# Optimization experiments

Measured on AMD Instinct MI355X. Metric: run time of the kernel, lower is better.

## Reference

```python
import jax, jax.numpy as jnp
import numpy as np

NY, NX = 1024, 2048
DX, DT, NU, UB = 1.0, 0.1, 0.01, 1.0
NITER = 5
NLEVEL = int(np.log2(NY)) + 1  # 11
DIAG = -8.0 / (3.0 * DX * DX)  # center coefficient of the Laplacian stencil wA


def _conv(x, w, stride=1):
    # single-channel 'VALID' cross-correlation, same semantics as torch Conv2d(padding=0)
    return jax.lax.conv_general_dilated(x, w, (stride, stride), 'VALID',
                                        dimension_numbers=('NCHW', 'OIHW', 'NCHW'))


def _bc_u(u):
    # inlet (left/top/bottom) = ub, zero-gradient outflow on the right
    uu = jnp.pad(u, ((0, 0), (0, 0), (1, 1), (1, 1)))
    uu = uu.at[:, :, :, 0].set(UB)
    uu = uu.at[:, :, :, -1].set(uu[:, :, :, -2])
    uu = uu.at[:, :, 0, :].set(UB)
    uu = uu.at[:, :, -1, :].set(UB)
    return uu


def _bc_v(v):
    # v = 0 on inlet/top/bottom (zero pad), zero-gradient outflow on the right
    vv = jnp.pad(v, ((0, 0), (0, 0), (1, 1), (1, 1)))
    vv = vv.at[:, :, :, -1].set(vv[:, :, :, -2])
    return vv


def _bc_p(p):
    # zero-gradient pressure except fixed p=0 at the outlet
    pp = jnp.pad(p, ((0, 0), (0, 0), (1, 1), (1, 1)))
    pp = pp.at[:, :, :, 0].set(pp[:, :, :, 1])
    pp = pp.at[:, :, :, -1].set(0.0)
    pp = pp.at[:, :, 0, :].set(pp[:, :, 1, :])
    pp = pp.at[:, :, -1, :].set(pp[:, :, -2, :])
    return pp


def _bc_cw(a):
    # homogeneous (zero) halo for the multigrid correction
    return jnp.pad(a, ((0, 0), (0, 0), (1, 1), (1, 1)))


def _prolong(a):
    return jnp.repeat(jnp.repeat(a, 2, axis=2), 2, axis=3)


def _f_cycle_mg(uu, vv, p, w_xadv, w_yadv, w_A, w_res):
    b = -(_conv(uu, w_xadv) + _conv(vv, w_yadv)) / DT
    for _ in range(NITER):
        r = _conv(_bc_p(p), w_A) - b
        r_s = [r]
        for _i in range(1, NLEVEL):
            r = _conv(r, w_res, stride=2)
            r_s.append(r)
        a = jnp.zeros((1, 1, 1, 1), dtype=p.dtype)
        for i in reversed(range(1, NLEVEL)):
            if i == NLEVEL - 1:
                a = r_s[i] / DIAG
            else:
                a = a - _conv(_bc_cw(a), w_A) / DIAG + r_s[i] / DIAG
            a = _prolong(a)
        p = p - a
        p = p - _conv(_bc_p(p), w_A) / DIAG + b / DIAG
    return p


def _forward(u, v, p, sigma, w_xadv, w_yadv, w_diff, w_A, w_res):
    uu, vv, pp = _bc_u(u), _bc_v(v), _bc_p(p)
    Grapx_p = _conv(pp, w_xadv) * DT
    Grapy_p = _conv(pp, w_yadv) * DT
    ADx_u, ADy_u = _conv(uu, w_xadv), _conv(uu, w_yadv)
    ADx_v, ADy_v = _conv(vv, w_xadv), _conv(vv, w_yadv)
    AD2_u, AD2_v = _conv(uu, w_diff), _conv(vv, w_diff)
    # predictor half-step
    bu = u + 0.5 * (NU * AD2_u * DT - u * ADx_u * DT - v * ADy_u * DT) - Grapx_p
    bv = v + 0.5 * (NU * AD2_v * DT - u * ADx_v * DT - v * ADy_v * DT) - Grapy_p
    damp = 1.0 / (1.0 + DT * sigma)  # solid body Brinkman penalty
    bu, bv = bu * damp, bv * damp
    buu, bvv = _bc_u(bu), _bc_v(bv)
    ADx_u, ADy_u = _conv(buu, w_xadv), _conv(buu, w_yadv)
    ADx_v, ADy_v = _conv(bvv, w_xadv), _conv(bvv, w_yadv)
    AD2_u, AD2_v = _conv(buu, w_diff), _conv(bvv, w_diff)
    # corrector step
    u = u + NU * AD2_u * DT - bu * ADx_u * DT - bv * ADy_u * DT - Grapx_p
    v = v + NU * AD2_v * DT - bu * ADx_v * DT - bv * ADy_v * DT - Grapy_p
    u, v = u * damp, v * damp
    uu, vv = _bc_u(u), _bc_v(v)
    # pressure solve via multigrid F-cycle + projection
    p = _f_cycle_mg(uu, vv, p, w_xadv, w_yadv, w_A, w_res)
    pp = _bc_p(p)
    u = u - _conv(pp, w_xadv) * DT
    v = v - _conv(pp, w_yadv) * DT
    u, v = u * damp, v * damp
    return jnp.concatenate([u, v, p], axis=1)  # (1, 3, NY, NX)


def setup_inputs() -> dict:
    key = jax.random.key(0)
    k1, k2, k3 = jax.random.split(key, 3)
    shp = (1, 1, NY, NX)
    u = jax.random.normal(k1, shp, jnp.float32) * 0.1 + UB
    v = jax.random.normal(k2, shp, jnp.float32) * 0.1
    p = jax.random.normal(k3, shp, jnp.float32) * 0.1
    # bluff-body mask: 1/timescale inside the rectangle (Block.create_solid_body_2D)
    cor_x, cor_y = NX // 4, NY // 2
    size_x, size_y = NX // 32, NY // 8
    sigma = jnp.zeros(shp, jnp.float32)
    sigma = sigma.at[0, 0, cor_y - size_y:cor_y + size_y,
                     cor_x - size_x:cor_x + size_x].set(1e8)
    # finite-difference stencils from get_weights_linear_2D(dx)
    w_diff = jnp.array([[1., 1., 1.], [1., -8., 1.], [1., 1., 1.]],
                       jnp.float32).reshape(1, 1, 3, 3) / (3.0 * DX * DX)
    w_xadv = jnp.array([[-1., 0., 1.], [-4., 0., 4.], [-1., 0., 1.]],
                       jnp.float32).reshape(1, 1, 3, 3) / (12.0 * DX)
    w_yadv = jnp.array([[-1., -4., -1.], [0., 0., 0.], [1., 4., 1.]],
                       jnp.float32).reshape(1, 1, 3, 3) / (12.0 * DX)
    w_A = w_diff
    w_res = jnp.full((1, 1, 2, 2), 0.25, jnp.float32)
    return {"u": u, "v": v, "p": p, "sigma": sigma, "w_xadv": w_xadv,
            "w_yadv": w_yadv, "w_diff": w_diff, "w_A": w_A, "w_res": w_res}


def reference(u, v, p, sigma, w_xadv, w_yadv, w_diff, w_A, w_res):
    return _forward(u, v, p, sigma, w_xadv, w_yadv, w_diff, w_A, w_res)
```

## Files before the change

### kernel.cpp

```cpp
#include <hip/hip_runtime.h>
#include <cstdint>

#define GNY 1024
#define GNX 2048
#define GNPTS (GNY * GNX)

namespace {
constexpr float DT = 0.1f;
constexpr float NUc = 0.01f;
constexpr float INV_DIAG = -0.375f;
}

__device__ __forceinline__ float bc_u_at(const float* __restrict__ f, int y, int x) {
    if (y < 0 || y >= GNY || x < 0) return 1.0f;
    if (x >= GNX) x = GNX - 1;
    return f[y * GNX + x];
}
__device__ __forceinline__ float bc_v_at(const float* __restrict__ f, int y, int x) {
    if (y < 0 || y >= GNY || x < 0) return 0.0f;
    if (x >= GNX) x = GNX - 1;
    return f[y * GNX + x];
}
__device__ __forceinline__ float bc_p_at(const float* __restrict__ f, int y, int x) {
    if (x >= GNX) return 0.0f;
    if (x < 0) x = 0;
    y = min(max(y, 0), GNY - 1);
    return f[y * GNX + x];
}

__device__ __forceinline__ float conv_x3(const float m[3][3]) {
    return ((m[0][2] - m[0][0]) + 4.0f * (m[1][2] - m[1][0]) + (m[2][2] - m[2][0])) * (1.0f / 12.0f);
}
__device__ __forceinline__ float conv_y3(const float m[3][3]) {
    return ((m[2][0] - m[0][0]) + 4.0f * (m[2][1] - m[0][1]) + (m[2][2] - m[0][2])) * (1.0f / 12.0f);
}
__device__ __forceinline__ float conv_d3(const float m[3][3]) {
    return (m[0][0] + m[0][1] + m[0][2] + m[1][0] + m[1][2] + m[2][0] + m[2][1] + m[2][2]
            - 8.0f * m[1][1]) * (1.0f / 3.0f);
}

template <typename PG>
__device__ __forceinline__ float up_val(PG pget, float rval, int H, int W, int y, int x) {
    float m[3][3];
#pragma unroll
    for (int dy = 0; dy < 3; ++dy)
#pragma unroll
        for (int dx = 0; dx < 3; ++dx) {
            int yy = y + dy - 1, xx = x + dx - 1;
            m[dy][dx] = (yy >= 0 && yy < H && xx >= 0 && xx < W) ? pget(yy >> 1, xx >> 1) : 0.0f;
        }
    float conv = (m[0][0] + m[0][1] + m[0][2] + m[1][0] + m[1][2]
                  + m[2][0] + m[2][1] + m[2][2] - 8.0f * m[1][1]) * (1.0f / 3.0f);
    return m[1][1] - conv * INV_DIAG + rval * INV_DIAG;
}

__global__ __launch_bounds__(256) void k_predict(
        const float* __restrict__ u, const float* __restrict__ v,
        const float* __restrict__ p, const float* __restrict__ sigma,
        float* __restrict__ bu, float* __restrict__ bv) {
    int x = blockIdx.x * blockDim.x + threadIdx.x;
    int y = blockIdx.y * blockDim.y + threadIdx.y;
    if (x >= GNX || y >= GNY) return;
    float un[3][3], vn[3][3], pn[3][3];
#pragma unroll
    for (int dy = 0; dy < 3; ++dy)
#pragma unroll
        for (int dx = 0; dx < 3; ++dx) {
            int yy = y + dy - 1, xx = x + dx - 1;
            un[dy][dx] = bc_u_at(u, yy, xx);
            vn[dy][dx] = bc_v_at(v, yy, xx);
            pn[dy][dx] = bc_p_at(p, yy, xx);
        }
    float gx = conv_x3(pn) * DT, gy = conv_y3(pn) * DT;
    float uc = un[1][1], vc = vn[1][1];
    float damp = 1.0f / (1.0f + DT * sigma[y * GNX + x]);
    float bu_ = uc + 0.5f * (NUc * conv_d3(un) * DT - uc * conv_x3(un) * DT - vc * conv_y3(un) * DT) - gx;
    float bv_ = vc + 0.5f * (NUc * conv_d3(vn) * DT - uc * conv_x3(vn) * DT - vc * conv_y3(vn) * DT) - gy;
    bu[y * GNX + x] = bu_ * damp;
    bv[y * GNX + x] = bv_ * damp;
}

__global__ __launch_bounds__(256) void k_correct(
        const float* __restrict__ u, const float* __restrict__ v,
        const float* __restrict__ p, const float* __restrict__ sigma,
        const float* __restrict__ bu, const float* __restrict__ bv,
        float* __restrict__ u2, float* __restrict__ v2) {
    int x = blockIdx.x * blockDim.x + threadIdx.x;
    int y = blockIdx.y * blockDim.y + threadIdx.y;
    if (x >= GNX || y >= GNY) return;
    float bun[3][3], bvn[3][3], pn[3][3];
#pragma unroll
    for (int dy = 0; dy < 3; ++dy)
#pragma unroll
        for (int dx = 0; dx < 3; ++dx) {
            int yy = y + dy - 1, xx = x + dx - 1;
            bun[dy][dx] = bc_u_at(bu, yy, xx);
            bvn[dy][dx] = bc_v_at(bv, yy, xx);
            pn[dy][dx] = bc_p_at(p, yy, xx);
        }
    float gx = conv_x3(pn) * DT, gy = conv_y3(pn) * DT;
    float buc = bun[1][1], bvc = bvn[1][1];
    int idx = y * GNX + x;
    float damp = 1.0f / (1.0f + DT * sigma[idx]);
    float un_ = u[idx] + NUc * conv_d3(bun) * DT - buc * conv_x3(bun) * DT - bvc * conv_y3(bun) * DT - gx;
    float vn_ = v[idx] + NUc * conv_d3(bvn) * DT - buc * conv_x3(bvn) * DT - bvc * conv_y3(bvn) * DT - gy;
    u2[idx] = un_ * damp;
    v2[idx] = vn_ * damp;
}

__global__ __launch_bounds__(256) void k_rhs(
        const float* __restrict__ u2, const float* __restrict__ v2, float* __restrict__ b) {
    int x = blockIdx.x * blockDim.x + threadIdx.x;
    int y = blockIdx.y * blockDim.y + threadIdx.y;
    if (x >= GNX || y >= GNY) return;
    float un[3][3], vn[3][3];
#pragma unroll
    for (int dy = 0; dy < 3; ++dy)
#pragma unroll
        for (int dx = 0; dx < 3; ++dx) {
            int yy = y + dy - 1, xx = x + dx - 1;
            un[dy][dx] = bc_u_at(u2, yy, xx);
            vn[dy][dx] = bc_v_at(v2, yy, xx);
        }
    b[y * GNX + x] = -(conv_x3(un) + conv_y3(vn)) * (1.0f / DT);
}

__global__ __launch_bounds__(256) void k_resid_restrict(
        const float* __restrict__ p, const float* __restrict__ b,
        float* __restrict__ r1, float* __restrict__ r2, float* __restrict__ r3,
        float* __restrict__ r4, float* __restrict__ r5) {
    __shared__ float s0[32][33];
    __shared__ float s1[16][17];
    __shared__ float s2[8][9];
    __shared__ float s3[4][5];
    __shared__ float s4[2][3];
    int t = threadIdx.x;
    int tx = t & 31, tg = t >> 5;
    int x0 = blockIdx.x * 32, y0 = blockIdx.y * 32;
    int x = x0 + tx;
#pragma unroll
    for (int ry = 0; ry < 4; ++ry) {
        int yr = tg * 4 + ry;
        int y = y0 + yr;
        float pn[3][3];
#pragma unroll
        for (int dy = 0; dy < 3; ++dy)
#pragma unroll
            for (int dx = 0; dx < 3; ++dx)
                pn[dy][dx] = bc_p_at(p, y + dy - 1, x + dx - 1);
        s0[yr][tx] = conv_d3(pn) - b[y * GNX + x];
    }
    __syncthreads();
    {   int qy = t >> 4, qx = t & 15;
        float v = 0.25f * (s0[2*qy][2*qx] + s0[2*qy][2*qx+1] + s0[2*qy+1][2*qx] + s0[2*qy+1][2*qx+1]);
        s1[qy][qx] = v;
        r1[(blockIdx.y * 16 + qy) * 1024 + blockIdx.x * 16 + qx] = v; }
    __syncthreads();
    if (t < 64) { int qy = t >> 3, qx = t & 7;
        float v = 0.25f * (s1[2*qy][2*qx] + s1[2*qy][2*qx+1] + s1[2*qy+1][2*qx] + s1[2*qy+1][2*qx+1]);
        s2[qy][qx] = v;
        r2[(blockIdx.y * 8 + qy) * 512 + blockIdx.x * 8 + qx] = v; }
    __syncthreads();
    if (t < 16) { int qy = t >> 2, qx = t & 3;
        float v = 0.25f * (s2[2*qy][2*qx] + s2[2*qy][2*qx+1] + s2[2*qy+1][2*qx] + s2[2*qy+1][2*qx+1]);
        s3[qy][qx] = v;
        r3[(blockIdx.y * 4 + qy) * 256 + blockIdx.x * 4 + qx] = v; }
    __syncthreads();
    if (t < 4) { int qy = t >> 1, qx = t & 1;
        float v = 0.25f * (s3[2*qy][2*qx] + s3[2*qy][2*qx+1] + s3[2*qy+1][2*qx] + s3[2*qy+1][2*qx+1]);
        s4[qy][qx] = v;
        r4[(blockIdx.y * 2 + qy) * 128 + blockIdx.x * 2 + qx] = v; }
    __syncthreads();
    if (t == 0)
        r5[blockIdx.y * 64 + blockIdx.x] = 0.25f * (s4[0][0] + s4[0][1] + s4[1][0] + s4[1][1]);
}

__global__ __launch_bounds__(256) void k_mg(
        const float* __restrict__ p_src, const float* __restrict__ b,
        const float* __restrict__ r1, const float* __restrict__ r2,
        const float* __restrict__ r3, const float* __restrict__ r4,
        const float* __restrict__ r5,
        float* __restrict__ p_dst,
        float* __restrict__ o1, float* __restrict__ o2, float* __restrict__ o3,
        float* __restrict__ o4, float* __restrict__ o5,
        const float* __restrict__ sigma, float* __restrict__ u_io,
        float* __restrict__ v_io, int last) {
    __shared__ float scr[3948];
    __shared__ float w6v[9], w5v[9], w4v[16], w3v[36], w2v[100], w1v[324];
    float* s5  = scr;
    float* s6  = scr + 2048;
    float* s7  = scr + 2560;
    float* s8  = scr + 2688;
    float* s9  = scr + 2720;
    float* s10 = scr + 2728;
    float* a9  = scr + 2730;
    float* a8  = scr + 2738;
    float* a7  = scr + 2770;
    float* sPp = scr;
    float* sPn = scr + 1332;
    float* s0  = scr + 2522;
    float* s1  = scr + 3578;
    float* s2  = scr + 3850;
    float* s3  = scr + 3922;
    float* s4  = scr + 3942;

    int t = threadIdx.x;
    int bx = blockIdx.x, by = blockIdx.y;
    int y0 = by * 32, x0 = bx * 32;

    for (int i = t; i < 2048; i += 256) s5[i] = r5[i];
    __syncthreads();
    for (int i = t; i < 512; i += 256) {
        int y = i >> 5, x = i & 31;
        s6[i] = 0.25f * (s5[(2*y)*64 + 2*x] + s5[(2*y)*64 + 2*x + 1]
                       + s5[(2*y+1)*64 + 2*x] + s5[(2*y+1)*64 + 2*x + 1]);
    }
    __syncthreads();
    if (t < 128) { int y = t >> 4, x = t & 15;
        s7[t] = 0.25f * (s6[(2*y)*32 + 2*x] + s6[(2*y)*32 + 2*x + 1]
                       + s6[(2*y+1)*32 + 2*x] + s6[(2*y+1)*32 + 2*x + 1]); }
    __syncthreads();
    if (t < 32) { int y = t >> 3, x = t & 7;
        s8[t] = 0.25f * (s7[(2*y)*16 + 2*x] + s7[(2*y)*16 + 2*x + 1]
                       + s7[(2*y+1)*16 + 2*x] + s7[(2*y+1)*16 + 2*x + 1]); }
    __syncthreads();
    if (t < 8) { int y = t >> 2, x = t & 3;
        s9[t] = 0.25f * (s8[(2*y)*8 + 2*x] + s8[(2*y)*8 + 2*x + 1]
                       + s8[(2*y+1)*8 + 2*x] + s8[(2*y+1)*8 + 2*x + 1]); }
    __syncthreads();
    if (t < 2)
        s10[t] = 0.25f * (s9[2*t] + s9[2*t + 1] + s9[4 + 2*t] + s9[4 + 2*t + 1]);
    __syncthreads();
    if (t < 8) { int y = t >> 2, x = t & 3;
        a9[t] = up_val([&](int py, int px) { return s10[py*2 + px] * INV_DIAG; },
                       s9[t], 2, 4, y, x); }
    __syncthreads();
    if (t < 32) { int y = t >> 3, x = t & 7;
        a8[t] = up_val([&](int py, int px) { return a9[py*4 + px]; },
                       s8[t], 4, 8, y, x); }
    __syncthreads();
    if (t < 128) { int y = t >> 4, x = t & 15;
        a7[t] = up_val([&](int py, int px) { return a8[py*8 + px]; },
                       s7[t], 8, 16, y, x); }
    __syncthreads();

    int w6ylo = (by - 2) >> 1, w6xlo = (bx - 2) >> 1;
    int w5ylo = by - 1,        w5xlo = bx - 1;
    int w4ylo = 2*by - 1,      w4xlo = 2*bx - 1;
    int w3ylo = 4*by - 1,      w3xlo = 4*bx - 1;
    int w2ylo = 8*by - 1,      w2xlo = 8*bx - 1;
    int w1ylo = 16*by - 1,     w1xlo = 16*bx - 1;

    if (t < 9) { int gy = w6ylo + t/3, gx = w6xlo + t%3;
        w6v[t] = (gy >= 0 && gy < 16 && gx >= 0 && gx < 32)
            ? up_val([&](int py, int px) { return a7[py*16 + px]; },
                     s6[gy*32 + gx], 16, 32, gy, gx) : 0.0f; }
    __syncthreads();
    if (t < 9) { int gy = w5ylo + t/3, gx = w5xlo + t%3;
        w5v[t] = (gy >= 0 && gy < 32 && gx >= 0 && gx < 64)
            ? up_val([&](int py, int px) { return w6v[(py - w6ylo)*3 + (px - w6xlo)]; },
                     s5[gy*64 + gx], 32, 64, gy, gx) : 0.0f; }
    __syncthreads();
    if (t < 16) { int gy = w4ylo + t/4, gx = w4xlo + t%4;
        w4v[t] = (gy >= 0 && gy < 64 && gx >= 0 && gx < 128)
            ? up_val([&](int py, int px) { return w5v[(py - w5ylo)*3 + (px - w5xlo)]; },
                     r4[gy*128 + gx], 64, 128, gy, gx) : 0.0f; }
    __syncthreads();
    if (t < 36) { int gy = w3ylo + t/6, gx = w3xlo + t%6;
        w3v[t] = (gy >= 0 && gy < 128 && gx >= 0 && gx < 256)
            ? up_val([&](int py, int px) { return w4v[(py - w4ylo)*4 + (px - w4xlo)]; },
                     r3[gy*256 + gx], 128, 256, gy, gx) : 0.0f; }
    __syncthreads();
    if (t < 100) { int gy = w2ylo + t/10, gx = w2xlo + t%10;
        w2v[t] = (gy >= 0 && gy < 256 && gx >= 0 && gx < 512)
            ? up_val([&](int py, int px) { return w3v[(py - w3ylo)*6 + (px - w3xlo)]; },
                     r2[gy*512 + gx], 256, 512, gy, gx) : 0.0f; }
    __syncthreads();
    for (int i = t; i < 324; i += 256) { int gy = w1ylo + i/18, gx = w1xlo + i%18;
        w1v[i] = (gy >= 0 && gy < 512 && gx >= 0 && gx < 1024)
            ? up_val([&](int py, int px) { return w2v[(py - w2ylo)*10 + (px - w2xlo)]; },
                     r1[gy*1024 + gx], 512, 1024, gy, gx) : 0.0f; }
    __syncthreads();

    for (int i = t; i < 1296; i += 256) {
        int wy = i / 36, wx = i % 36;
        int gy = y0 - 2 + wy, gx = x0 - 2 + wx;
        float v = 0.0f;
        if (gy >= 0 && gy < GNY && gx >= 0 && gx < GNX)
            v = p_src[gy*GNX + gx] - w1v[((gy >> 1) - w1ylo)*18 + ((gx >> 1) - w1xlo)];
        sPp[wy*37 + wx] = v;
    }
    __syncthreads();
    for (int i = t; i < 1156; i += 256) {
        int wy = i / 34, wx = i % 34;
        int gy = y0 - 1 + wy, gx = x0 - 1 + wx;
        float v = 0.0f;
        if (gy >= 0 && gy < GNY && gx >= 0 && gx < GNX) {
            float m[3][3];
#pragma unroll
            for (int dy = 0; dy < 3; ++dy)
#pragma unroll
                for (int dx = 0; dx < 3; ++dx) {
                    int yy = gy + dy - 1, xx = gx + dx - 1;
                    float tv;
                    if (xx >= GNX) tv = 0.0f;
                    else {
                        int cx = xx < 0 ? 0 : xx;
                        int cy = min(max(yy, 0), GNY - 1);
                        tv = sPp[(cy - (y0 - 2))*37 + (cx - (x0 - 2))];
                    }
                    m[dy][dx] = tv;
                }
            float conv = (m[0][0] + m[0][1] + m[0][2] + m[1][0] + m[1][2]
                          + m[2][0] + m[2][1] + m[2][2] - 8.0f*m[1][1]) * (1.0f / 3.0f);
            v = m[1][1] - conv * INV_DIAG + b[gy*GNX + gx] * INV_DIAG;
        }
        sPn[wy*35 + wx] = v;
    }
    __syncthreads();
    for (int i = t; i < 1024; i += 256) {
        int ty = i >> 5, tx = i & 31;
        p_dst[(y0 + ty)*GNX + x0 + tx] = sPn[(ty + 1)*35 + (tx + 1)];
    }

    if (!last) {
        for (int i = t; i < 1024; i += 256) {
            int ty = i >> 5, tx = i & 31;
            int gy = y0 + ty, gx = x0 + tx;
            float m[3][3];
#pragma unroll
            for (int dy = 0; dy < 3; ++dy)
#pragma unroll
                for (int dx = 0; dx < 3; ++dx) {
                    int yy = gy + dy - 1, xx = gx + dx - 1;
                    float tv;
                    if (xx >= GNX) tv = 0.0f;
                    else {
                        int cx = xx < 0 ? 0 : xx;
                        int cy = min(max(yy, 0), GNY - 1);
                        tv = sPn[(cy - (y0 - 1))*35 + (cx - (x0 - 1))];
                    }
                    m[dy][dx] = tv;
                }
            s0[ty*33 + tx] = conv_d3(m) - b[gy*GNX + gx];
        }
        __syncthreads();
        { int qy = t >> 4, qx = t & 15;
          float v = 0.25f * (s0[(2*qy)*33 + 2*qx] + s0[(2*qy)*33 + 2*qx + 1]
                           + s0[(2*qy+1)*33 + 2*qx] + s0[(2*qy+1)*33 + 2*qx + 1]);
          s1[qy*17 + qx] = v;
          o1[(by*16 + qy)*1024 + bx*16 + qx] = v; }
        __syncthreads();
        if (t < 64) { int qy = t >> 3, qx = t & 7;
          float v = 0.25f * (s1[(2*qy)*17 + 2*qx] + s1[(2*qy)*17 + 2*qx + 1]
                           + s1[(2*qy+1)*17 + 2*qx] + s1[(2*qy+1)*17 + 2*qx + 1]);
          s2[qy*9 + qx] = v;
          o2[(by*8 + qy)*512 + bx*8 + qx] = v; }
        __syncthreads();
        if (t < 16) { int qy = t >> 2, qx = t & 3;
          float v = 0.25f * (s2[(2*qy)*9 + 2*qx] + s2[(2*qy)*9 + 2*qx + 1]
                           + s2[(2*qy+1)*9 + 2*qx] + s2[(2*qy+1)*9 + 2*qx + 1]);
          s3[qy*5 + qx] = v;
          o3[(by*4 + qy)*256 + bx*4 + qx] = v; }
        __syncthreads();
        if (t < 4) { int qy = t >> 1, qx = t & 1;
          float v = 0.25f * (s3[(2*qy)*5 + 2*qx] + s3[(2*qy)*5 + 2*qx + 1]
                           + s3[(2*qy+1)*5 + 2*qx] + s3[(2*qy+1)*5 + 2*qx + 1]);
          s4[qy*3 + qx] = v;
          o4[(by*2 + qy)*128 + bx*2 + qx] = v; }
        __syncthreads();
        if (t == 0)
            o5[by*64 + bx] = 0.25f * (s4[0] + s4[1] + s4[3] + s4[4]);
    } else {
        for (int i = t; i < 1024; i += 256) {
            int ty = i >> 5, tx = i & 31;
            int gy = y0 + ty, gx = x0 + tx;
            float m[3][3];
#pragma unroll
            for (int dy = 0; dy < 3; ++dy)
#pragma unroll
                for (int dx = 0; dx < 3; ++dx) {
                    int yy = gy + dy - 1, xx = gx + dx - 1;
                    float tv;
                    if (xx >= GNX) tv = 0.0f;
                    else {
                        int cx = xx < 0 ? 0 : xx;
                        int cy = min(max(yy, 0), GNY - 1);
                        tv = sPn[(cy - (y0 - 1))*35 + (cx - (x0 - 1))];
                    }
                    m[dy][dx] = tv;
                }
            int idx = gy*GNX + gx;
            float damp = 1.0f / (1.0f + DT * sigma[idx]);
            u_io[idx] = (u_io[idx] - conv_x3(m) * DT) * damp;
            v_io[idx] = (v_io[idx] - conv_y3(m) * DT) * damp;
        }
    }
}

extern "C" void kernel_launch(void* const* d_in, const int* in_sizes, int n_in,
                              void* d_out, int out_size, void* d_ws, size_t ws_size,
                              hipStream_t stream) {
    (void)in_sizes; (void)n_in; (void)out_size; (void)ws_size;
    const float* u_in  = (const float*)d_in[0];
    const float* v_in  = (const float*)d_in[1];
    const float* p_in  = (const float*)d_in[2];
    const float* sigma = (const float*)d_in[3];

    float* out_u = (float*)d_out;
    float* out_v = out_u + GNPTS;
    float* out_p = out_u + 2 * (size_t)GNPTS;

    float* ws   = (float*)d_ws;
    float* bu   = ws;
    float* bv   = bu + (size_t)GNPTS;
    float* b    = bv + (size_t)GNPTS;
    float* p_ws = b  + (size_t)GNPTS;
    float* base = p_ws + (size_t)GNPTS;
    float* A_[5], * B_[5];
    size_t lsz[5] = {524288, 131072, 32768, 8192, 2048};
    float* cur = base;
    for (int l = 0; l < 5; ++l) { A_[l] = cur; cur += lsz[l]; }
    for (int l = 0; l < 5; ++l) { B_[l] = cur; cur += lsz[l]; }

    dim3 blk2(64, 4), grd2(GNX / 64, GNY / 4);
    dim3 grdT(GNX / 32, GNY / 32), blkT(256);

    k_predict<<<grd2, blk2, 0, stream>>>(u_in, v_in, p_in, sigma, bu, bv);
    k_correct<<<grd2, blk2, 0, stream>>>(u_in, v_in, p_in, sigma, bu, bv, out_u, out_v);
    k_rhs<<<grd2, blk2, 0, stream>>>(out_u, out_v, b);

    k_resid_restrict<<<grdT, blkT, 0, stream>>>(p_in, b, A_[0], A_[1], A_[2], A_[3], A_[4]);

    const float* p_cur = p_in;
    float* p_bufs[2] = { out_p, p_ws };
    for (int it = 0; it < 5; ++it) {
        float** rp = (it % 2 == 0) ? A_ : B_;
        float** wp = (it % 2 == 0) ? B_ : A_;
        float* p_next = p_bufs[it % 2];
        int last = (it == 4) ? 1 : 0;
        k_mg<<<grdT, blkT, 0, stream>>>(p_cur, b,
                                        rp[0], rp[1], rp[2], rp[3], rp[4],
                                        p_next,
                                        wp[0], wp[1], wp[2], wp[3], wp[4],
                                        sigma, out_u, out_v, last);
        p_cur = p_next;
    }
}
```

Before: 239.0 us.

## Fuse predictor, corrector, RHS and restriction into one halo-recompute kernel

Merges the four front-end kernels (predict, correct, divergence RHS, residual+restriction) into a single tiled kernel. Each 32x32 tile recomputes bu/bv on a 2-cell halo and u2/v2 on a 1-cell halo in shared memory, so the bu/bv intermediates never touch global memory and three launches are dropped. The cost is redundant halo computation (about 27% extra for bu/bv) and heavy shared-memory use that may reduce occupancy.

Measured after the change: 240.3 us. No clear change (+0.5%).

```diff
diff --git a/kernel.cpp b/kernel.cpp
--- a/kernel.cpp
+++ b/kernel.cpp
@@ -54,125 +54,138 @@
     return m[1][1] - conv * INV_DIAG + rval * INV_DIAG;
 }
 
-__global__ __launch_bounds__(256) void k_predict(
+__global__ __launch_bounds__(256) void k_front(
         const float* __restrict__ u, const float* __restrict__ v,
         const float* __restrict__ p, const float* __restrict__ sigma,
-        float* __restrict__ bu, float* __restrict__ bv) {
-    int x = blockIdx.x * blockDim.x + threadIdx.x;
-    int y = blockIdx.y * blockDim.y + threadIdx.y;
-    if (x >= GNX || y >= GNY) return;
-    float un[3][3], vn[3][3], pn[3][3];
-#pragma unroll
-    for (int dy = 0; dy < 3; ++dy)
-#pragma unroll
-        for (int dx = 0; dx < 3; ++dx) {
-            int yy = y + dy - 1, xx = x + dx - 1;
-            un[dy][dx] = bc_u_at(u, yy, xx);
-            vn[dy][dx] = bc_v_at(v, yy, xx);
-            pn[dy][dx] = bc_p_at(p, yy, xx);
-        }
-    float gx = conv_x3(pn) * DT, gy = conv_y3(pn) * DT;
-    float uc = un[1][1], vc = vn[1][1];
-    float damp = 1.0f / (1.0f + DT * sigma[y * GNX + x]);
-    float bu_ = uc + 0.5f * (NUc * conv_d3(un) * DT - uc * conv_x3(un) * DT - vc * conv_y3(un) * DT) - gx;
-    float bv_ = vc + 0.5f * (NUc * conv_d3(vn) * DT - uc * conv_x3(vn) * DT - vc * conv_y3(vn) * DT) - gy;
-    bu[y * GNX + x] = bu_ * damp;
-    bv[y * GNX + x] = bv_ * damp;
-}
-
-__global__ __launch_bounds__(256) void k_correct(
-        const float* __restrict__ u, const float* __restrict__ v,
-        const float* __restrict__ p, const float* __restrict__ sigma,
-        const float* __restrict__ bu, const float* __restrict__ bv,
-        float* __restrict__ u2, float* __restrict__ v2) {
-    int x = blockIdx.x * blockDim.x + threadIdx.x;
-    int y = blockIdx.y * blockDim.y + threadIdx.y;
-    if (x >= GNX || y >= GNY) return;
-    float bun[3][3], bvn[3][3], pn[3][3];
-#pragma unroll
-    for (int dy = 0; dy < 3; ++dy)
-#pragma unroll
-        for (int dx = 0; dx < 3; ++dx) {
-            int yy = y + dy - 1, xx = x + dx - 1;
-            bun[dy][dx] = bc_u_at(bu, yy, xx);
-            bvn[dy][dx] = bc_v_at(bv, yy, xx);
-            pn[dy][dx] = bc_p_at(p, yy, xx);
-        }
-    float gx = conv_x3(pn) * DT, gy = conv_y3(pn) * DT;
-    float buc = bun[1][1], bvc = bvn[1][1];
-    int idx = y * GNX + x;
-    float damp = 1.0f / (1.0f + DT * sigma[idx]);
-    float un_ = u[idx] + NUc * conv_d3(bun) * DT - buc * conv_x3(bun) * DT - bvc * conv_y3(bun) * DT - gx;
-    float vn_ = v[idx] + NUc * conv_d3(bvn) * DT - buc * conv_x3(bvn) * DT - bvc * conv_y3(bvn) * DT - gy;
-    u2[idx] = un_ * damp;
-    v2[idx] = vn_ * damp;
-}
-
-__global__ __launch_bounds__(256) void k_rhs(
-        const float* __restrict__ u2, const float* __restrict__ v2, float* __restrict__ b) {
-    int x = blockIdx.x * blockDim.x + threadIdx.x;
-    int y = blockIdx.y * blockDim.y + threadIdx.y;
-    if (x >= GNX || y >= GNY) return;
-    float un[3][3], vn[3][3];
-#pragma unroll
-    for (int dy = 0; dy < 3; ++dy)
-#pragma unroll
-        for (int dx = 0; dx < 3; ++dx) {
-            int yy = y + dy - 1, xx = x + dx - 1;
-            un[dy][dx] = bc_u_at(u2, yy, xx);
-            vn[dy][dx] = bc_v_at(v2, yy, xx);
-        }
-    b[y * GNX + x] = -(conv_x3(un) + conv_y3(vn)) * (1.0f / DT);
-}
-
-__global__ __launch_bounds__(256) void k_resid_restrict(
-        const float* __restrict__ p, const float* __restrict__ b,
+        float* __restrict__ u2g, float* __restrict__ v2g, float* __restrict__ bg,
         float* __restrict__ r1, float* __restrict__ r2, float* __restrict__ r3,
         float* __restrict__ r4, float* __restrict__ r5) {
-    __shared__ float s0[32][33];
-    __shared__ float s1[16][17];
-    __shared__ float s2[8][9];
-    __shared__ float s3[4][5];
-    __shared__ float s4[2][3];
+    __shared__ float sBu[36 * 37], sBv[36 * 37];
+    __shared__ float sU2[34 * 35], sV2[34 * 35];
+    __shared__ float s0[32 * 33];
+    __shared__ float s1[16 * 17];
+    __shared__ float s2[8 * 9];
+    __shared__ float s3[4 * 5];
+    __shared__ float s4[2 * 3];
+
     int t = threadIdx.x;
-    int tx = t & 31, tg = t >> 5;
-    int x0 = blockIdx.x * 32, y0 = blockIdx.y * 32;
-    int x = x0 + tx;
-#pragma unroll
-    for (int ry = 0; ry < 4; ++ry) {
-        int yr = tg * 4 + ry;
-        int y = y0 + yr;
-        float pn[3][3];
+    int bx = blockIdx.x, by = blockIdx.y;
+    int y0 = by * 32, x0 = bx * 32;
+
+    for (int i = t; i < 1296; i += 256) {
+        int wy = i / 36, wx = i - wy * 36;
+        int gy = y0 - 2 + wy, gx = x0 - 2 + wx;
+        float bu_ = 0.0f, bv_ = 0.0f;
+        if (gy >= 0 && gy < GNY && gx >= 0 && gx < GNX) {
+            float un[3][3], vn[3][3], pn[3][3];
+#pragma unroll
+            for (int dy = 0; dy < 3; ++dy)
+#pragma unroll
+                for (int dx = 0; dx < 3; ++dx) {
+                    int yy = gy + dy - 1, xx = gx + dx - 1;
+                    un[dy][dx] = bc_u_at(u, yy, xx);
+                    vn[dy][dx] = bc_v_at(v, yy, xx);
+                    pn[dy][dx] = bc_p_at(p, yy, xx);
+                }
+            float gxp = conv_x3(pn) * DT, gyp = conv_y3(pn) * DT;
+            float uc = un[1][1], vc = vn[1][1];
+            float damp = 1.0f / (1.0f + DT * sigma[gy * GNX + gx]);
+            bu_ = (uc + 0.5f * (NUc * conv_d3(un) * DT - uc * conv_x3(un) * DT - vc * conv_y3(un) * DT) - gxp) * damp;
+            bv_ = (vc + 0.5f * (NUc * conv_d3(vn) * DT - uc * conv_x3(vn) * DT - vc * conv_y3(vn) * DT) - gyp) * damp;
+        }
+        sBu[wy * 37 + wx] = bu_;
+        sBv[wy * 37 + wx] = bv_;
+    }
+    __syncthreads();
+
+    for (int i = t; i < 1156; i += 256) {
+        int wy = i / 34, wx = i - wy * 34;
+        int gy = y0 - 1 + wy, gx = x0 - 1 + wx;
+        float u2_ = 0.0f, v2_ = 0.0f;
+        if (gy >= 0 && gy < GNY && gx >= 0 && gx < GNX) {
+            float bun[3][3], bvn[3][3], pn[3][3];
+#pragma unroll
+            for (int dy = 0; dy < 3; ++dy)
+#pragma unroll
+                for (int dx = 0; dx < 3; ++dx) {
+                    int yy = gy + dy - 1, xx = gx + dx - 1;
+                    float buv, bvv;
+                    if (yy < 0 || yy >= GNY || xx < 0) { buv = 1.0f; bvv = 0.0f; }
+                    else {
+                        int cx = (xx >= GNX) ? GNX - 1 : xx;
+                        int li = (yy - (y0 - 2)) * 37 + (cx - (x0 - 2));
+                        buv = sBu[li]; bvv = sBv[li];
+                    }
+                    bun[dy][dx] = buv; bvn[dy][dx] = bvv;
+                    pn[dy][dx] = bc_p_at(p, yy, xx);
+                }
+            float gxp = conv_x3(pn) * DT, gyp = conv_y3(pn) * DT;
+            float buc = bun[1][1], bvc = bvn[1][1];
+            int idx = gy * GNX + gx;
+            float damp = 1.0f / (1.0f + DT * sigma[idx]);
+            u2_ = (u[idx] + NUc * conv_d3(bun) * DT - buc * conv_x3(bun) * DT - bvc * conv_y3(bun) * DT - gxp) * damp;
+            v2_ = (v[idx] + NUc * conv_d3(bvn) * DT - buc * conv_x3(bvn) * DT - bvc * conv_y3(bvn) * DT - gyp) * damp;
+            if (wy >= 1 && wy <= 32 && wx >= 1 && wx <= 32) {
+                u2g[idx] = u2_;
+                v2g[idx] = v2_;
+            }
+        }
+        sU2[wy * 35 + wx] = u2_;
+        sV2[wy * 35 + wx] = v2_;
+    }
+    __syncthreads();
+
+    for (int i = t; i < 1024; i += 256) {
+        int ty = i >> 5, tx = i & 31;
+        int gy = y0 + ty, gx = x0 + tx;
+        float un[3][3], vn[3][3], pn[3][3];
 #pragma unroll
         for (int dy = 0; dy < 3; ++dy)
 #pragma unroll
-            for (int dx = 0; dx < 3; ++dx)
-                pn[dy][dx] = bc_p_at(p, y + dy - 1, x + dx - 1);
-        s0[yr][tx] = conv_d3(pn) - b[y * GNX + x];
-    }
-    __syncthreads();
-    {   int qy = t >> 4, qx = t & 15;
-        float v = 0.25f * (s0[2*qy][2*qx] + s0[2*qy][2*qx+1] + s0[2*qy+1][2*qx] + s0[2*qy+1][2*qx+1]);
-        s1[qy][qx] = v;
-        r1[(blockIdx.y * 16 + qy) * 1024 + blockIdx.x * 16 + qx] = v; }
+            for (int dx = 0; dx < 3; ++dx) {
+                int yy = gy + dy - 1, xx = gx + dx - 1;
+                float uv, vv;
+                if (yy < 0 || yy >= GNY || xx < 0) { uv = 1.0f; vv = 0.0f; }
+                else {
+                    int cx = (xx >= GNX) ? GNX - 1 : xx;
+                    int li = (yy - (y0 - 1)) * 35 + (cx - (x0 - 1));
+                    uv = sU2[li]; vv = sV2[li];
+                }
+                un[dy][dx] = uv; vn[dy][dx] = vv;
+                pn[dy][dx] = bc_p_at(p, yy, xx);
+            }
+        float b_ = -(conv_x3(un) + conv_y3(vn)) * (1.0f / DT);
+        bg[gy * GNX + gx] = b_;
+        s0[ty * 33 + tx] = conv_d3(pn) - b_;
+    }
+    __syncthreads();
+
+    { int qy = t >> 4, qx = t & 15;
+      float vv = 0.25f * (s0[(2*qy)*33 + 2*qx] + s0[(2*qy)*33 + 2*qx + 1]
+                        + s0[(2*qy+1)*33 + 2*qx] + s0[(2*qy+1)*33 + 2*qx + 1]);
+      s1[qy*17 + qx] = vv;
+      r1[(by*16 + qy)*1024 + bx*16 + qx] = vv; }
     __syncthreads();
     if (t < 64) { int qy = t >> 3, qx = t & 7;
-        float v = 0.25f * (s1[2*qy][2*qx] + s1[2*qy][2*qx+1] + s1[2*qy+1][2*qx] + s1[2*qy+1][2*qx+1]);
-        s2[qy][qx] = v;
-        r2[(blockIdx.y * 8 + qy) * 512 + blockIdx.x * 8 + qx] = v; }
+      float vv = 0.25f * (s1[(2*qy)*17 + 2*qx] + s1[(2*qy)*17 + 2*qx + 1]
+                        + s1[(2*qy+1)*17 + 2*qx] + s1[(2*qy+1)*17 + 2*qx + 1]);
+      s2[qy*9 + qx] = vv;
+      r2[(by*8 + qy)*512 + bx*8 + qx] = vv; }
     __syncthreads();
     if (t < 16) { int qy = t >> 2, qx = t & 3;
-        float v = 0.25f * (s2[2*qy][2*qx] + s2[2*qy][2*qx+1] + s2[2*qy+1][2*qx] + s2[2*qy+1][2*qx+1]);
-        s3[qy][qx] = v;
-        r3[(blockIdx.y * 4 + qy) * 256 + blockIdx.x * 4 + qx] = v; }
+      float vv = 0.25f * (s2[(2*qy)*9 + 2*qx] + s2[(2*qy)*9 + 2*qx + 1]
+                        + s2[(2*qy+1)*9 + 2*qx] + s2[(2*qy+1)*9 + 2*qx + 1]);
+      s3[qy*5 + qx] = vv;
+      r3[(by*4 + qy)*256 + bx*4 + qx] = vv; }
     __syncthreads();
     if (t < 4) { int qy = t >> 1, qx = t & 1;
-        float v = 0.25f * (s3[2*qy][2*qx] + s3[2*qy][2*qx+1] + s3[2*qy+1][2*qx] + s3[2*qy+1][2*qx+1]);
-        s4[qy][qx] = v;
-        r4[(blockIdx.y * 2 + qy) * 128 + blockIdx.x * 2 + qx] = v; }
+      float vv = 0.25f * (s3[(2*qy)*5 + 2*qx] + s3[(2*qy)*5 + 2*qx + 1]
+                        + s3[(2*qy+1)*5 + 2*qx] + s3[(2*qy+1)*5 + 2*qx + 1]);
+      s4[qy*3 + qx] = vv;
+      r4[(by*2 + qy)*128 + bx*2 + qx] = vv; }
     __syncthreads();
     if (t == 0)
-        r5[blockIdx.y * 64 + blockIdx.x] = 0.25f * (s4[0][0] + s4[0][1] + s4[1][0] + s4[1][1]);
+        r5[by*64 + bx] = 0.25f * (s4[0] + s4[1] + s4[3] + s4[4]);
 }
 
 __global__ __launch_bounds__(256) void k_mg(
@@ -412,10 +425,8 @@
     float* out_p = out_u + 2 * (size_t)GNPTS;
 
     float* ws   = (float*)d_ws;
-    float* bu   = ws;
-    float* bv   = bu + (size_t)GNPTS;
-    float* b    = bv + (size_t)GNPTS;
-    float* p_ws = b  + (size_t)GNPTS;
+    float* b    = ws;
+    float* p_ws = b + (size_t)GNPTS;
     float* base = p_ws + (size_t)GNPTS;
     float* A_[5], * B_[5];
     size_t lsz[5] = {524288, 131072, 32768, 8192, 2048};
@@ -423,14 +434,11 @@
     for (int l = 0; l < 5; ++l) { A_[l] = cur; cur += lsz[l]; }
     for (int l = 0; l < 5; ++l) { B_[l] = cur; cur += lsz[l]; }
 
-    dim3 blk2(64, 4), grd2(GNX / 64, GNY / 4);
     dim3 grdT(GNX / 32, GNY / 32), blkT(256);
 
-    k_predict<<<grd2, blk2, 0, stream>>>(u_in, v_in, p_in, sigma, bu, bv);
-    k_correct<<<grd2, blk2, 0, stream>>>(u_in, v_in, p_in, sigma, bu, bv, out_u, out_v);
-    k_rhs<<<grd2, blk2, 0, stream>>>(out_u, out_v, b);
-
-    k_resid_restrict<<<grdT, blkT, 0, stream>>>(p_in, b, A_[0], A_[1], A_[2], A_[3], A_[4]);
+    k_front<<<grdT, blkT, 0, stream>>>(u_in, v_in, p_in, sigma,
+                                       out_u, out_v, b,
+                                       A_[0], A_[1], A_[2], A_[3], A_[4]);
 
     const float* p_cur = p_in;
     float* p_bufs[2] = { out_p, p_ws };
```
